# Kernel optimization log

Measured on AMD Instinct MI355X. Metric: run time of the kernel, lower is better.

## Reference

```python
import jax, jax.numpy as jnp
import numpy as np

D_MODEL = 1024
H = 16
D_K = D_MODEL // H
NEG = -1e9


def setup_inputs() -> dict:
    key = jax.random.key(0)
    ks = jax.random.split(key, 8)
    B, S = 4, 2048
    q = jax.random.normal(ks[0], (B, S, D_MODEL), dtype=jnp.float32)
    k = jax.random.normal(ks[1], (B, S, D_MODEL), dtype=jnp.float32)
    v = jax.random.normal(ks[2], (B, S, D_MODEL), dtype=jnp.float32)
    mask = jax.random.randint(ks[3], (B, S), 0, 2, dtype=jnp.int32)
    scale = 1.0 / np.sqrt(D_MODEL)
    Wq = jax.random.normal(ks[4], (D_MODEL, D_MODEL), dtype=jnp.float32) * scale
    Wk = jax.random.normal(ks[5], (D_MODEL, D_MODEL), dtype=jnp.float32) * scale
    Wv = jax.random.normal(ks[6], (D_MODEL, D_MODEL), dtype=jnp.float32) * scale
    Wo = jax.random.normal(ks[7], (D_MODEL, D_MODEL), dtype=jnp.float32) * scale
    return {"q": q, "k": k, "v": v, "mask": mask,
            "Wq": Wq, "Wk": Wk, "Wv": Wv, "Wo": Wo}


def _split_heads(x):
    # [B,S,d_model] -> [B,H,S,d_k]
    B, S, _ = x.shape
    return x.reshape(B, S, H, D_K).transpose(0, 2, 1, 3)


def reference(q, k, v, mask, Wq, Wk, Wv, Wo):
    # Linear projections (torch Linear: x @ W.T, no bias)
    query = _split_heads(jnp.einsum('bsd,ed->bse', q, Wq))
    key_ = _split_heads(jnp.einsum('bsd,ed->bse', k, Wk))
    value = _split_heads(jnp.einsum('bsd,ed->bse', v, Wv))
    # scaled dot-product attention, manual path
    scores = jnp.einsum('bhqd,bhkd->bhqk', query, key_) / jnp.sqrt(
        jnp.asarray(D_K, dtype=query.dtype))
    m = (mask == 0)[:, None, None, :]  # [B,1,1,S]
    scores = jnp.where(m, jnp.asarray(NEG, dtype=scores.dtype), scores)
    attn = jax.nn.softmax(scores, axis=-1)
    mh = jnp.einsum('bhqk,bhkd->bhqd', attn, value)
    # merge heads -> [B,S,d_model]
    B = mh.shape[0]
    mh = mh.transpose(0, 2, 1, 3).reshape(B, -1, D_MODEL)
    return jnp.einsum('bsd,ed->bse', mh, Wo)
```

## Files before the change

### kernel.cpp

```cpp
#include <hip/hip_runtime.h>
#include <math.h>

typedef __attribute__((ext_vector_type(4))) float f32x4;
typedef __attribute__((ext_vector_type(8))) __bf16 bf16x8;
typedef __attribute__((ext_vector_type(2))) __bf16 bf16x2;

#ifndef __has_builtin
#define __has_builtin(x) 0
#endif

#if __has_builtin(__builtin_amdgcn_exp2f)
#define EXP2F(x) __builtin_amdgcn_exp2f(x)
#else
#define EXP2F(x) exp2f(x)
#endif

__device__ __forceinline__ ushort f2bf(float f) {
  return (ushort)((__float_as_uint(f) + 0x8000u) >> 16);
}

__device__ __forceinline__ uint pack_bf16(float a, float b) {
#if __has_builtin(__builtin_amdgcn_cvt_pk_bf16_f32)
  bf16x2 p = __builtin_amdgcn_cvt_pk_bf16_f32(a, b);
  return __builtin_bit_cast(uint, p);
#elif __has_builtin(__builtin_amdgcn_perm)
  uint au = __float_as_uint(a) + 0x8000u;
  uint bu = __float_as_uint(b) + 0x8000u;
  return __builtin_amdgcn_perm(bu, au, 0x07060302u);
#else
  return (uint)f2bf(a) | ((uint)f2bf(b) << 16);
#endif
}

__device__ __forceinline__ void async_cp16(const void* g, void* l) {
  __builtin_amdgcn_global_load_lds(
      (const __attribute__((address_space(1))) void*)g,
      (__attribute__((address_space(3))) void*)l, 16, 0, 0);
}


__global__ __launch_bounds__(256) void bias_kernel(const int* __restrict__ mask,
                                                   float* __restrict__ bias) {
  int i = blockIdx.x * 256 + threadIdx.x;
  bias[i] = mask[i] ? 0.0f : -1e9f;
}

__global__ __launch_bounds__(256) void cast3_kernel(const float* __restrict__ q,
                                                    const float* __restrict__ k,
                                                    const float* __restrict__ v,
                                                    ushort* qo, ushort* ko, ushort* vo) {
  int y = blockIdx.y;
  const float* in = y == 0 ? q : (y == 1 ? k : v);
  ushort* out = y == 0 ? qo : (y == 1 ? ko : vo);
  int i = blockIdx.x * 256 + threadIdx.x;
  float4 f = ((const float4*)in)[i];
  uint2 o;
  o.x = pack_bf16(f.x, f.y);
  o.y = pack_bf16(f.z, f.w);
  ((uint2*)out)[i] = o;
}

__global__ __launch_bounds__(256) void cast4_kernel(const float* __restrict__ a,
                                                    const float* __restrict__ b,
                                                    const float* __restrict__ c,
                                                    const float* __restrict__ d,
                                                    ushort* ao, ushort* bo, ushort* co, ushort* do_) {
  int y = blockIdx.y;
  const float* in = y == 0 ? a : (y == 1 ? b : (y == 2 ? c : d));
  ushort* out = y == 0 ? ao : (y == 1 ? bo : (y == 2 ? co : do_));
  int i = blockIdx.x * 256 + threadIdx.x;
  float4 f = ((const float4*)in)[i];
  uint2 o;
  o.x = pack_bf16(f.x, f.y);
  o.y = pack_bf16(f.z, f.w);
  ((uint2*)out)[i] = o;
}


__device__ __forceinline__ void gemm_body(const ushort* __restrict__ A,
                                          const ushort* __restrict__ W,
                                          void* __restrict__ Cout, int mode) {
  constexpr int N = 1024, K = 1024;
  __shared__ ushort As[128 * 32];
  __shared__ ushort Bs[128 * 32];
  const int bm = blockIdx.y * 128;
  const int bn = blockIdx.x * 128;
  const int tid = threadIdx.x;
  const int w = tid >> 6, lane = tid & 63;
  const int g = lane >> 4, cc = lane & 15;
  const int wm = (w >> 1) * 64, wn = (w & 1) * 64;

  f32x4 acc[4][4];
#pragma unroll
  for (int i = 0; i < 4; ++i)
#pragma unroll
    for (int j = 0; j < 4; ++j) acc[i][j] = (f32x4)0.0f;

  for (int k0 = 0; k0 < K; k0 += 32) {
#pragma unroll
    for (int j = 0; j < 2; ++j) {
      int cbase = w * 128 + j * 64;
      int cid = cbase + lane;
      int row = cid & 127, kb = cid >> 7;
      async_cp16(A + (size_t)(bm + row) * K + k0 + kb * 8, &As[cbase * 8]);
      async_cp16(W + (size_t)(bn + row) * K + k0 + kb * 8, &Bs[cbase * 8]);
    }
    __syncthreads();
    bf16x8 af[4], bfr[4];
#pragma unroll
    for (int mi = 0; mi < 4; ++mi)
      af[mi] = *(const bf16x8*)&As[(g * 128 + wm + mi * 16 + cc) * 8];
#pragma unroll
    for (int ni = 0; ni < 4; ++ni)
      bfr[ni] = *(const bf16x8*)&Bs[(g * 128 + wn + ni * 16 + cc) * 8];
#pragma unroll
    for (int mi = 0; mi < 4; ++mi)
#pragma unroll
      for (int ni = 0; ni < 4; ++ni)
        acc[mi][ni] = __builtin_amdgcn_mfma_f32_16x16x32_bf16(af[mi], bfr[ni], acc[mi][ni], 0, 0, 0);
    __syncthreads();
  }

  const float qsc = 0.18033688011112042f;
#pragma unroll
  for (int mi = 0; mi < 4; ++mi) {
#pragma unroll
    for (int ni = 0; ni < 4; ++ni) {
#pragma unroll
      for (int r = 0; r < 4; ++r) {
        int row = bm + wm + mi * 16 + g * 4 + r;
        int col = bn + wn + ni * 16 + cc;
        float val = acc[mi][ni][r];
        if (mode == 0) {
          ((ushort*)Cout)[(size_t)row * N + col] = f2bf(val);
        } else if (mode == 1) {
          ((float*)Cout)[(size_t)row * N + col] = val;
        } else if (mode == 3) {
          ((ushort*)Cout)[(size_t)row * N + col] = f2bf(val * qsc);
        } else {
          int b = row >> 11, s = row & 2047;
          int h = col >> 6, d = col & 63;
          ((ushort*)Cout)[(size_t)((b * 16 + h) * 64 + d) * 2048 + s] = f2bf(val);
        }
      }
    }
  }
}

__global__ __launch_bounds__(256) void qkv_gemm_kernel(const ushort* qb, const ushort* kb,
                                                       const ushort* vb, const ushort* wq,
                                                       const ushort* wk, const ushort* wv,
                                                       ushort* Qp, ushort* Kp, ushort* Vt) {
  int z = blockIdx.z;
  const ushort* A = z == 0 ? qb : (z == 1 ? kb : vb);
  const ushort* W = z == 0 ? wq : (z == 1 ? wk : wv);
  void* C = z == 0 ? (void*)Qp : (z == 1 ? (void*)Kp : (void*)Vt);
  gemm_body(A, W, C, z == 2 ? 2 : (z == 0 ? 3 : 0));
}

__global__ __launch_bounds__(256) void gemm1_kernel(const ushort* A, const ushort* W,
                                                    void* C, int mode) {
  gemm_body(A, W, C, mode);
}

__global__ __launch_bounds__(256, 4) void attn_kernel(const ushort* __restrict__ Qp,
                                                      const ushort* __restrict__ Kp,
                                                      const ushort* __restrict__ Vt,
                                                      const float* __restrict__ bias,
                                                      ushort* __restrict__ mh) {
  constexpr int S = 2048, DM = 1024, DK = 64;
  __shared__ ushort k_lds[64 * 64];
  __shared__ ushort v_lds[64 * 64];
  __shared__ ushort pt_lds[4 * 2176];

  const int bh = blockIdx.x;
  const int qt = blockIdx.y;
  const int b = bh >> 4, h = bh & 15;
  const int tid = threadIdx.x;
  const int w = tid >> 6, lane = tid & 63;
  const int g = lane >> 4, cc = lane & 15;
  ushort* ptw = &pt_lds[w * 2176];

  const int q0 = qt * 128 + w * 32;
  bf16x8 qf[2][2];
#pragma unroll
  for (int ni = 0; ni < 2; ++ni) {
    size_t row = (size_t)(b * S + q0 + ni * 16 + cc);
#pragma unroll
    for (int ks = 0; ks < 2; ++ks)
      qf[ks][ni] = *(const bf16x8*)&Qp[row * DM + h * DK + ks * 32 + g * 8];
  }

  bf16x8 ones;
#pragma unroll
  for (int i = 0; i < 8; ++i) ones[i] = (__bf16)1.0f;

  f32x4 o_acc[4][2];
#pragma unroll
  for (int i = 0; i < 4; ++i)
#pragma unroll
    for (int j = 0; j < 2; ++j) o_acc[i][j] = (f32x4)0.0f;
  f32x4 l_acc[2] = {(f32x4)0.0f, (f32x4)0.0f};
  float m_i[2] = {-3e38f, -3e38f};
  const float* biasb = bias + b * S;

  for (int kt = 0; kt < S / 64; ++kt) {
    if (kt) __syncthreads();
#pragma unroll
    for (int j = 0; j < 2; ++j) {
      int cb = j * 256 + w * 64;
      int cid = cb + lane;
      async_cp16(Kp + (size_t)(b * S + kt * 64 + (cid & 63)) * DM + h * DK + (cid >> 6) * 8,
                 &k_lds[cb * 8]);
      async_cp16(Vt + (size_t)(bh * DK + (cid & 63)) * S + kt * 64 + (cid >> 6) * 8,
                 &v_lds[cb * 8]);
    }
    __syncthreads();

    f32x4 sacc[4][2];
#pragma unroll
    for (int mi = 0; mi < 4; ++mi)
#pragma unroll
      for (int ni = 0; ni < 2; ++ni) sacc[mi][ni] = (f32x4)0.0f;
#pragma unroll
    for (int ks = 0; ks < 2; ++ks)
#pragma unroll
      for (int mi = 0; mi < 4; ++mi) {
        bf16x8 kf = *(const bf16x8*)&k_lds[((ks * 4 + g) * 64 + mi * 16 + cc) * 8];
        sacc[mi][0] = __builtin_amdgcn_mfma_f32_16x16x32_bf16(kf, qf[ks][0], sacc[mi][0], 0, 0, 0);
        sacc[mi][1] = __builtin_amdgcn_mfma_f32_16x16x32_bf16(kf, qf[ks][1], sacc[mi][1], 0, 0, 0);
      }

    float mx[2] = {-3e38f, -3e38f};
#pragma unroll
    for (int mi = 0; mi < 4; ++mi) {
      float4 bv = *(const float4*)&biasb[kt * 64 + mi * 16 + g * 4];
      const float* bvp = &bv.x;
#pragma unroll
      for (int r = 0; r < 4; ++r) {
#pragma unroll
        for (int ni = 0; ni < 2; ++ni) {
          float t = sacc[mi][ni][r] + bvp[r];
          sacc[mi][ni][r] = t;
          mx[ni] = fmaxf(mx[ni], t);
        }
      }
    }
    float mn[2];
#pragma unroll
    for (int ni = 0; ni < 2; ++ni) {
      float m = mx[ni];
      m = fmaxf(m, __shfl_xor(m, 16, 64));
      m = fmaxf(m, __shfl_xor(m, 32, 64));
      mn[ni] = fmaxf(m_i[ni], m);
      float al = EXP2F(m_i[ni] - mn[ni]);
      m_i[ni] = mn[ni];
      l_acc[ni][0] *= al;
#pragma unroll
      for (int md = 0; md < 4; ++md)
#pragma unroll
        for (int r = 0; r < 4; ++r) o_acc[md][ni][r] *= al;
    }

#pragma unroll
    for (int mi = 0; mi < 4; ++mi)
#pragma unroll
      for (int ni = 0; ni < 2; ++ni) {
        float p0 = EXP2F(sacc[mi][ni][0] - mn[ni]);
        float p1 = EXP2F(sacc[mi][ni][1] - mn[ni]);
        float p2 = EXP2F(sacc[mi][ni][2] - mn[ni]);
        float p3 = EXP2F(sacc[mi][ni][3] - mn[ni]);
        uint2 pv;
        pv.x = pack_bf16(p0, p1);
        pv.y = pack_bf16(p2, p3);
        int base = ((mi * 2 + (g >> 1)) * 32 + ni * 16 + cc) * 8 + (g & 1) * 4;
        *(uint2*)&ptw[base] = pv;
      }

#pragma unroll
    for (int ks = 0; ks < 2; ++ks) {
      bf16x8 ptf[2];
#pragma unroll
      for (int ni = 0; ni < 2; ++ni)
        ptf[ni] = *(const bf16x8*)&ptw[((ks * 4 + g) * 32 + ni * 16 + cc) * 8];
      l_acc[0] = __builtin_amdgcn_mfma_f32_16x16x32_bf16(ones, ptf[0], l_acc[0], 0, 0, 0);
      l_acc[1] = __builtin_amdgcn_mfma_f32_16x16x32_bf16(ones, ptf[1], l_acc[1], 0, 0, 0);
#pragma unroll
      for (int md = 0; md < 4; ++md) {
        bf16x8 vf = *(const bf16x8*)&v_lds[((ks * 4 + g) * 64 + md * 16 + cc) * 8];
        o_acc[md][0] = __builtin_amdgcn_mfma_f32_16x16x32_bf16(vf, ptf[0], o_acc[md][0], 0, 0, 0);
        o_acc[md][1] = __builtin_amdgcn_mfma_f32_16x16x32_bf16(vf, ptf[1], o_acc[md][1], 0, 0, 0);
      }
    }
  }

  float rl[2];
#pragma unroll
  for (int ni = 0; ni < 2; ++ni) rl[ni] = 1.0f / l_acc[ni][0];

#pragma unroll
  for (int md = 0; md < 4; ++md)
#pragma unroll
    for (int ni = 0; ni < 2; ++ni) {
      int ql = ni * 16 + cc;
      int dbase = md * 16 + g * 4;
      *(uint*)&ptw[ql * 68 + dbase] =
          pack_bf16(o_acc[md][ni][0] * rl[ni], o_acc[md][ni][1] * rl[ni]);
      *(uint*)&ptw[ql * 68 + dbase + 2] =
          pack_bf16(o_acc[md][ni][2] * rl[ni], o_acc[md][ni][3] * rl[ni]);
    }
#pragma unroll
  for (int pass = 0; pass < 4; ++pass) {
    int ql = pass * 8 + (lane >> 3);
    int dc = lane & 7;
    uint4 val = *(const uint4*)&ptw[ql * 68 + dc * 8];
    *(uint4*)&mh[(size_t)(b * S + q0 + ql) * DM + h * DK + dc * 8] = val;
  }
}


extern "C" void kernel_launch(void* const* d_in, const int* in_sizes, int n_in,
                              void* d_out, int out_size, void* d_ws, size_t ws_size,
                              hipStream_t stream) {
  const float* q = (const float*)d_in[0];
  const float* k = (const float*)d_in[1];
  const float* v = (const float*)d_in[2];
  const int* mask = (const int*)d_in[3];
  const float* Wq = (const float*)d_in[4];
  const float* Wk = (const float*)d_in[5];
  const float* Wv = (const float*)d_in[6];
  const float* Wo = (const float*)d_in[7];

  const int M = 8192, Dm = 1024;
  const size_t MB = 1 << 20;

  char* ws = (char*)d_ws;
  ushort* Qp = (ushort*)(ws);
  ushort* Kp = (ushort*)(ws + 16 * MB);
  ushort* Vt = (ushort*)(ws + 32 * MB);
  ushort* wqb = (ushort*)(ws + 48 * MB);
  ushort* wkb = wqb + (1 << 20);
  ushort* wvb = wkb + (1 << 20);
  ushort* wob = wvb + (1 << 20);
  float* biasbuf = (float*)(ws + 56 * MB);
  ushort* vb = (ushort*)(ws + 57 * MB);
  ushort* mh = vb;
  ushort* qb = (ushort*)d_out;
  ushort* kb = qb + (size_t)8 * 1024 * 1024;

  dim3 blk(256);
  dim3 ggrid(Dm / 128, M / 128);

  cast4_kernel<<<dim3(1024, 4), blk, 0, stream>>>(Wq, Wk, Wv, Wo, wqb, wkb, wvb, wob);
  bias_kernel<<<dim3(32), blk, 0, stream>>>(mask, biasbuf);
  cast3_kernel<<<dim3(8192, 3), blk, 0, stream>>>(q, k, v, qb, kb, vb);
  qkv_gemm_kernel<<<dim3(Dm / 128, M / 128, 3), blk, 0, stream>>>(qb, kb, vb, wqb, wkb, wvb,
                                                                  Qp, Kp, Vt);
  attn_kernel<<<dim3(64, 16), blk, 0, stream>>>(Qp, Kp, Vt, biasbuf, mh);
  gemm1_kernel<<<ggrid, blk, 0, stream>>>(mh, wob, d_out, 1);
}
```

Before: 445.8 us.

## Fuse fp32-to-bf16 activation cast into QKV GEMM loads and swizzle block order

Drops the separate cast kernel for q/k/v. The QKV GEMM now reads fp32 activations directly, converts them to bf16 in registers and stores them to LDS, which removes a full write and re-read of the bf16 copies. Both GEMMs also remap block indices so that neighbouring blocks share A-row tiles, aiming for better L2 reuse. In exchange the A operand is now loaded synchronously through registers instead of with async global-to-LDS copies, so the GEMM main loop may stall more on memory latency.

Result: slower. 480.4 us (+7.8%).

```diff
diff --git a/kernel.cpp b/kernel.cpp
--- a/kernel.cpp
+++ b/kernel.cpp
@@ -43,21 +43,6 @@
                                                    float* __restrict__ bias) {
   int i = blockIdx.x * 256 + threadIdx.x;
   bias[i] = mask[i] ? 0.0f : -1e9f;
-}
-
-__global__ __launch_bounds__(256) void cast3_kernel(const float* __restrict__ q,
-                                                    const float* __restrict__ k,
-                                                    const float* __restrict__ v,
-                                                    ushort* qo, ushort* ko, ushort* vo) {
-  int y = blockIdx.y;
-  const float* in = y == 0 ? q : (y == 1 ? k : v);
-  ushort* out = y == 0 ? qo : (y == 1 ? ko : vo);
-  int i = blockIdx.x * 256 + threadIdx.x;
-  float4 f = ((const float4*)in)[i];
-  uint2 o;
-  o.x = pack_bf16(f.x, f.y);
-  o.y = pack_bf16(f.z, f.w);
-  ((uint2*)out)[i] = o;
 }
 
 __global__ __launch_bounds__(256) void cast4_kernel(const float* __restrict__ a,
@@ -77,14 +62,14 @@
 }
 
 
-__device__ __forceinline__ void gemm_body(const ushort* __restrict__ A,
+template <bool AFP32>
+__device__ __forceinline__ void gemm_body(const void* __restrict__ Ain,
                                           const ushort* __restrict__ W,
-                                          void* __restrict__ Cout, int mode) {
+                                          void* __restrict__ Cout, int mode,
+                                          int bm, int bn) {
   constexpr int N = 1024, K = 1024;
   __shared__ ushort As[128 * 32];
   __shared__ ushort Bs[128 * 32];
-  const int bm = blockIdx.y * 128;
-  const int bn = blockIdx.x * 128;
   const int tid = threadIdx.x;
   const int w = tid >> 6, lane = tid & 63;
   const int g = lane >> 4, cc = lane & 15;
@@ -96,14 +81,38 @@
 #pragma unroll
     for (int j = 0; j < 4; ++j) acc[i][j] = (f32x4)0.0f;
 
+  const int arow = tid & 127, akb = tid >> 7;
+  const float* aptr = AFP32 ? (const float*)Ain + (size_t)(bm + arow) * K + akb * 8 : nullptr;
+  const ushort* Ab = (const ushort*)Ain;
+
   for (int k0 = 0; k0 < K; k0 += 32) {
 #pragma unroll
-    for (int j = 0; j < 2; ++j) {
-      int cbase = w * 128 + j * 64;
+    for (int jj = 0; jj < 2; ++jj) {
+      int cbase = w * 128 + jj * 64;
       int cid = cbase + lane;
       int row = cid & 127, kb = cid >> 7;
-      async_cp16(A + (size_t)(bm + row) * K + k0 + kb * 8, &As[cbase * 8]);
       async_cp16(W + (size_t)(bn + row) * K + k0 + kb * 8, &Bs[cbase * 8]);
+    }
+    if (AFP32) {
+      float4 a0 = *(const float4*)(aptr + k0);
+      float4 a1 = *(const float4*)(aptr + k0 + 4);
+      float4 a2 = *(const float4*)(aptr + k0 + 16);
+      float4 a3 = *(const float4*)(aptr + k0 + 20);
+      uint4 c0, c1;
+      c0.x = pack_bf16(a0.x, a0.y); c0.y = pack_bf16(a0.z, a0.w);
+      c0.z = pack_bf16(a1.x, a1.y); c0.w = pack_bf16(a1.z, a1.w);
+      c1.x = pack_bf16(a2.x, a2.y); c1.y = pack_bf16(a2.z, a2.w);
+      c1.z = pack_bf16(a3.x, a3.y); c1.w = pack_bf16(a3.z, a3.w);
+      *(uint4*)&As[(size_t)tid * 8] = c0;
+      *(uint4*)&As[(size_t)(tid + 256) * 8] = c1;
+    } else {
+#pragma unroll
+      for (int jj = 0; jj < 2; ++jj) {
+        int cbase = w * 128 + jj * 64;
+        int cid = cbase + lane;
+        int row = cid & 127, kb = cid >> 7;
+        async_cp16(Ab + (size_t)(bm + row) * K + k0 + kb * 8, &As[cbase * 8]);
+      }
     }
     __syncthreads();
     bf16x8 af[4], bfr[4];
@@ -147,20 +156,27 @@
   }
 }
 
-__global__ __launch_bounds__(256) void qkv_gemm_kernel(const ushort* qb, const ushort* kb,
-                                                       const ushort* vb, const ushort* wq,
+__global__ __launch_bounds__(256) void qkv_gemm_kernel(const float* q, const float* k,
+                                                       const float* v, const ushort* wq,
                                                        const ushort* wk, const ushort* wv,
                                                        ushort* Qp, ushort* Kp, ushort* Vt) {
-  int z = blockIdx.z;
-  const ushort* A = z == 0 ? qb : (z == 1 ? kb : vb);
+  int lid = blockIdx.x + (blockIdx.y << 3) + (blockIdx.z << 9);
+  int j = lid & 7, s = lid >> 3;
+  int x = s & 7, yl = (s >> 3) & 7, z = s >> 6;
+  int y = (j << 3) | yl;
+  const float* A = z == 0 ? q : (z == 1 ? k : v);
   const ushort* W = z == 0 ? wq : (z == 1 ? wk : wv);
   void* C = z == 0 ? (void*)Qp : (z == 1 ? (void*)Kp : (void*)Vt);
-  gemm_body(A, W, C, z == 2 ? 2 : (z == 0 ? 3 : 0));
-}
-
-__global__ __launch_bounds__(256) void gemm1_kernel(const ushort* A, const ushort* W,
-                                                    void* C, int mode) {
-  gemm_body(A, W, C, mode);
+  gemm_body<true>(A, W, C, z == 2 ? 2 : (z == 0 ? 3 : 0), y * 128, x * 128);
+}
+
+__global__ __launch_bounds__(256) void gemm_wo_kernel(const ushort* A, const ushort* W,
+                                                      float* C) {
+  int lid = blockIdx.x + (blockIdx.y << 3);
+  int j = lid & 7, s = lid >> 3;
+  int x = s & 7, yl = s >> 3;
+  int y = (j << 3) | yl;
+  gemm_body<false>(A, W, C, 1, y * 128, x * 128);
 }
 
 __global__ __launch_bounds__(256, 4) void attn_kernel(const ushort* __restrict__ Qp,
@@ -331,7 +347,7 @@
   const float* Wv = (const float*)d_in[6];
   const float* Wo = (const float*)d_in[7];
 
-  const int M = 8192, Dm = 1024;
+  const int Dm = 1024;
   const size_t MB = 1 << 20;
 
   char* ws = (char*)d_ws;
@@ -343,19 +359,13 @@
   ushort* wvb = wkb + (1 << 20);
   ushort* wob = wvb + (1 << 20);
   float* biasbuf = (float*)(ws + 56 * MB);
-  ushort* vb = (ushort*)(ws + 57 * MB);
-  ushort* mh = vb;
-  ushort* qb = (ushort*)d_out;
-  ushort* kb = qb + (size_t)8 * 1024 * 1024;
+  ushort* mh = (ushort*)(ws + 57 * MB);
 
   dim3 blk(256);
-  dim3 ggrid(Dm / 128, M / 128);
 
   cast4_kernel<<<dim3(1024, 4), blk, 0, stream>>>(Wq, Wk, Wv, Wo, wqb, wkb, wvb, wob);
   bias_kernel<<<dim3(32), blk, 0, stream>>>(mask, biasbuf);
-  cast3_kernel<<<dim3(8192, 3), blk, 0, stream>>>(q, k, v, qb, kb, vb);
-  qkv_gemm_kernel<<<dim3(Dm / 128, M / 128, 3), blk, 0, stream>>>(qb, kb, vb, wqb, wkb, wvb,
-                                                                  Qp, Kp, Vt);
+  qkv_gemm_kernel<<<dim3(8, 64, 3), blk, 0, stream>>>(q, k, v, wqb, wkb, wvb, Qp, Kp, Vt);
   attn_kernel<<<dim3(64, 16), blk, 0, stream>>>(Qp, Kp, Vt, biasbuf, mh);
-  gemm1_kernel<<<ggrid, blk, 0, stream>>>(mh, wob, d_out, 1);
-}
+  gemm_wo_kernel<<<dim3(8, 64), blk, 0, stream>>>(mh, wob, (float*)d_out);
+}
```

## Fuse cast/bias prep kernels and double GEMM K-tile to 64

Applied to the files above, without the earlier changes.

Merges the three prep kernels (weight cast, input cast, mask-to-bias) into one launch to cut launch overhead. The GEMM body now stages 64-wide K tiles instead of 32, halving barrier pairs per K loop and doing two MFMA sub-steps per tile. It also specialises the output GEMM kernel for fp32 output. The larger LDS tiles double shared memory per block, which may lower occupancy, and the loads are still not double-buffered.

Measured after the change: 436.1 us. 2.2% less time.

```diff
diff --git a/kernel.cpp b/kernel.cpp
--- a/kernel.cpp
+++ b/kernel.cpp
@@ -39,52 +39,50 @@
 }
 
 
-__global__ __launch_bounds__(256) void bias_kernel(const int* __restrict__ mask,
-                                                   float* __restrict__ bias) {
-  int i = blockIdx.x * 256 + threadIdx.x;
-  bias[i] = mask[i] ? 0.0f : -1e9f;
-}
-
-__global__ __launch_bounds__(256) void cast3_kernel(const float* __restrict__ q,
-                                                    const float* __restrict__ k,
-                                                    const float* __restrict__ v,
-                                                    ushort* qo, ushort* ko, ushort* vo) {
-  int y = blockIdx.y;
-  const float* in = y == 0 ? q : (y == 1 ? k : v);
-  ushort* out = y == 0 ? qo : (y == 1 ? ko : vo);
-  int i = blockIdx.x * 256 + threadIdx.x;
-  float4 f = ((const float4*)in)[i];
-  uint2 o;
-  o.x = pack_bf16(f.x, f.y);
-  o.y = pack_bf16(f.z, f.w);
-  ((uint2*)out)[i] = o;
-}
-
-__global__ __launch_bounds__(256) void cast4_kernel(const float* __restrict__ a,
-                                                    const float* __restrict__ b,
-                                                    const float* __restrict__ c,
-                                                    const float* __restrict__ d,
-                                                    ushort* ao, ushort* bo, ushort* co, ushort* do_) {
-  int y = blockIdx.y;
-  const float* in = y == 0 ? a : (y == 1 ? b : (y == 2 ? c : d));
-  ushort* out = y == 0 ? ao : (y == 1 ? bo : (y == 2 ? co : do_));
-  int i = blockIdx.x * 256 + threadIdx.x;
-  float4 f = ((const float4*)in)[i];
-  uint2 o;
-  o.x = pack_bf16(f.x, f.y);
-  o.y = pack_bf16(f.z, f.w);
-  ((uint2*)out)[i] = o;
+__global__ __launch_bounds__(256) void prep_kernel(
+    const float* __restrict__ q, const float* __restrict__ k, const float* __restrict__ v,
+    const float* __restrict__ Wq, const float* __restrict__ Wk, const float* __restrict__ Wv,
+    const float* __restrict__ Wo, const int* __restrict__ mask,
+    ushort* qb, ushort* kb, ushort* vb,
+    ushort* wqb, ushort* wkb, ushort* wvb, ushort* wob,
+    float* bias) {
+  int b = blockIdx.x;
+  int tid = threadIdx.x;
+  if (b < 4096) {
+    int j = b >> 10;
+    const float* in = j == 0 ? Wq : (j == 1 ? Wk : (j == 2 ? Wv : Wo));
+    ushort* out = j == 0 ? wqb : (j == 1 ? wkb : (j == 2 ? wvb : wob));
+    int i = (b & 1023) * 256 + tid;
+    float4 f = ((const float4*)in)[i];
+    uint2 o;
+    o.x = pack_bf16(f.x, f.y);
+    o.y = pack_bf16(f.z, f.w);
+    ((uint2*)out)[i] = o;
+  } else if (b < 28672) {
+    int bb = b - 4096;
+    int j = bb >> 13;
+    const float* in = j == 0 ? q : (j == 1 ? k : v);
+    ushort* out = j == 0 ? qb : (j == 1 ? kb : vb);
+    int i = (bb & 8191) * 256 + tid;
+    float4 f = ((const float4*)in)[i];
+    uint2 o;
+    o.x = pack_bf16(f.x, f.y);
+    o.y = pack_bf16(f.z, f.w);
+    ((uint2*)out)[i] = o;
+  } else {
+    int i = (b - 28672) * 256 + tid;
+    bias[i] = mask[i] ? 0.0f : -1e9f;
+  }
 }
 
 
 __device__ __forceinline__ void gemm_body(const ushort* __restrict__ A,
                                           const ushort* __restrict__ W,
-                                          void* __restrict__ Cout, int mode) {
+                                          void* __restrict__ Cout, int mode,
+                                          int bm, int bn) {
   constexpr int N = 1024, K = 1024;
-  __shared__ ushort As[128 * 32];
-  __shared__ ushort Bs[128 * 32];
-  const int bm = blockIdx.y * 128;
-  const int bn = blockIdx.x * 128;
+  __shared__ ushort As[128 * 64];
+  __shared__ ushort Bs[128 * 64];
   const int tid = threadIdx.x;
   const int w = tid >> 6, lane = tid & 63;
   const int g = lane >> 4, cc = lane & 15;
@@ -96,29 +94,40 @@
 #pragma unroll
     for (int j = 0; j < 4; ++j) acc[i][j] = (f32x4)0.0f;
 
-  for (int k0 = 0; k0 < K; k0 += 32) {
-#pragma unroll
-    for (int j = 0; j < 2; ++j) {
-      int cbase = w * 128 + j * 64;
+  auto stage = [&](int k0) {
+#pragma unroll
+    for (int j = 0; j < 4; ++j) {
+      int cbase = w * 256 + j * 64;
       int cid = cbase + lane;
       int row = cid & 127, kb = cid >> 7;
       async_cp16(A + (size_t)(bm + row) * K + k0 + kb * 8, &As[cbase * 8]);
       async_cp16(W + (size_t)(bn + row) * K + k0 + kb * 8, &Bs[cbase * 8]);
     }
+  };
+
+  stage(0);
+  for (int it = 0; it < K / 64; ++it) {
     __syncthreads();
-    bf16x8 af[4], bfr[4];
-#pragma unroll
-    for (int mi = 0; mi < 4; ++mi)
-      af[mi] = *(const bf16x8*)&As[(g * 128 + wm + mi * 16 + cc) * 8];
-#pragma unroll
-    for (int ni = 0; ni < 4; ++ni)
-      bfr[ni] = *(const bf16x8*)&Bs[(g * 128 + wn + ni * 16 + cc) * 8];
-#pragma unroll
-    for (int mi = 0; mi < 4; ++mi)
+#pragma unroll
+    for (int ks = 0; ks < 2; ++ks) {
+      bf16x8 af[4], bfr[4];
+#pragma unroll
+      for (int mi = 0; mi < 4; ++mi)
+        af[mi] = *(const bf16x8*)&As[((ks * 4 + g) * 128 + wm + mi * 16 + cc) * 8];
 #pragma unroll
       for (int ni = 0; ni < 4; ++ni)
-        acc[mi][ni] = __builtin_amdgcn_mfma_f32_16x16x32_bf16(af[mi], bfr[ni], acc[mi][ni], 0, 0, 0);
-    __syncthreads();
+        bfr[ni] = *(const bf16x8*)&Bs[((ks * 4 + g) * 128 + wn + ni * 16 + cc) * 8];
+#pragma unroll
+      for (int mi = 0; mi < 4; ++mi)
+#pragma unroll
+        for (int ni = 0; ni < 4; ++ni)
+          acc[mi][ni] =
+              __builtin_amdgcn_mfma_f32_16x16x32_bf16(af[mi], bfr[ni], acc[mi][ni], 0, 0, 0);
+    }
+    if (it < K / 64 - 1) {
+      __syncthreads();
+      stage((it + 1) * 64);
+    }
   }
 
   const float qsc = 0.18033688011112042f;
@@ -155,12 +164,12 @@
   const ushort* A = z == 0 ? qb : (z == 1 ? kb : vb);
   const ushort* W = z == 0 ? wq : (z == 1 ? wk : wv);
   void* C = z == 0 ? (void*)Qp : (z == 1 ? (void*)Kp : (void*)Vt);
-  gemm_body(A, W, C, z == 2 ? 2 : (z == 0 ? 3 : 0));
-}
-
-__global__ __launch_bounds__(256) void gemm1_kernel(const ushort* A, const ushort* W,
-                                                    void* C, int mode) {
-  gemm_body(A, W, C, mode);
+  gemm_body(A, W, C, z == 2 ? 2 : (z == 0 ? 3 : 0), blockIdx.y * 128, blockIdx.x * 128);
+}
+
+__global__ __launch_bounds__(256) void gemm_wo_kernel(const ushort* A, const ushort* W,
+                                                      float* C) {
+  gemm_body(A, W, C, 1, blockIdx.y * 128, blockIdx.x * 128);
 }
 
 __global__ __launch_bounds__(256, 4) void attn_kernel(const ushort* __restrict__ Qp,
@@ -331,7 +340,6 @@
   const float* Wv = (const float*)d_in[6];
   const float* Wo = (const float*)d_in[7];
 
-  const int M = 8192, Dm = 1024;
   const size_t MB = 1 << 20;
 
   char* ws = (char*)d_ws;
@@ -349,13 +357,10 @@
   ushort* kb = qb + (size_t)8 * 1024 * 1024;
 
   dim3 blk(256);
-  dim3 ggrid(Dm / 128, M / 128);
-
-  cast4_kernel<<<dim3(1024, 4), blk, 0, stream>>>(Wq, Wk, Wv, Wo, wqb, wkb, wvb, wob);
-  bias_kernel<<<dim3(32), blk, 0, stream>>>(mask, biasbuf);
-  cast3_kernel<<<dim3(8192, 3), blk, 0, stream>>>(q, k, v, qb, kb, vb);
-  qkv_gemm_kernel<<<dim3(Dm / 128, M / 128, 3), blk, 0, stream>>>(qb, kb, vb, wqb, wkb, wvb,
-                                                                  Qp, Kp, Vt);
+
+  prep_kernel<<<dim3(28704), blk, 0, stream>>>(q, k, v, Wq, Wk, Wv, Wo, mask,
+                                               qb, kb, vb, wqb, wkb, wvb, wob, biasbuf);
+  qkv_gemm_kernel<<<dim3(8, 64, 3), blk, 0, stream>>>(qb, kb, vb, wqb, wkb, wvb, Qp, Kp, Vt);
   attn_kernel<<<dim3(64, 16), blk, 0, stream>>>(Qp, Kp, Vt, biasbuf, mh);
-  gemm1_kernel<<<ggrid, blk, 0, stream>>>(mh, wob, d_out, 1);
-}
+  gemm_wo_kernel<<<dim3(8, 64), blk, 0, stream>>>(mh, wob, (float*)d_out);
+}
```
